# Performance work log

Measured on AMD Instinct MI355X. Metric: run time of the kernel, lower is better.

Reference implementation:

```python
import jax, jax.numpy as jnp
import numpy as np

H = 128
L = 3
N = 100000
E = 1600000
G = 1024
OUT = 10
MAX_LEVEL = 1000
MAX_THOUGHTS = 5000
N_CATE = 5
BN_EPS = 1e-5


def _make_pe(n_pos, h):
    pos = np.arange(n_pos, dtype=np.float32)[:, None]
    div = np.exp(np.arange(0, h, 2, dtype=np.float32) * (-np.log(10000.0) / h))
    pe = np.zeros((n_pos, h), dtype=np.float32)
    pe[:, 0::2] = np.sin(pos * div)
    pe[:, 1::2] = np.cos(pos * div)
    return jnp.asarray(pe)


def setup_inputs() -> dict:
    key = jax.random.key(0)
    ks = jax.random.split(key, 16)
    s = 0.02
    inp = {
        "x": jax.random.randint(ks[0], (N, 3), 0, 5, dtype=jnp.int64 if jax.config.jax_enable_x64 else jnp.int32),
        "edge_index": jax.random.randint(ks[1], (2, E), 0, N),
        "batch": jnp.sort(jax.random.randint(ks[2], (N,), 0, G)),
        "num_graphs": G,
        "pe": _make_pe(MAX_THOUGHTS, H),
        "cate_emb": jax.random.normal(ks[3], (N_CATE, H), jnp.float32) * s,
        "level_emb": jax.random.normal(ks[4], (MAX_LEVEL, H), jnp.float32) * s,
        "conv_W1": jax.random.normal(ks[5], (L, H, H), jnp.float32) * s,
        "conv_b1": jnp.zeros((L, H), jnp.float32),
        "conv_g1": jnp.ones((L, H), jnp.float32),
        "conv_be1": jnp.zeros((L, H), jnp.float32),
        "conv_W2": jax.random.normal(ks[6], (L, H, H), jnp.float32) * s,
        "conv_b2": jnp.zeros((L, H), jnp.float32),
        "norm_g": jnp.ones((L, H), jnp.float32),
        "norm_be": jnp.zeros((L, H), jnp.float32),
        "gate_W1": jax.random.normal(ks[7], (H, H), jnp.float32) * s,
        "gate_b1": jnp.zeros((H,), jnp.float32),
        "gate_W2": jax.random.normal(ks[8], (H, 1), jnp.float32) * s,
        "gate_b2": jnp.zeros((1,), jnp.float32),
        "cls_W1": jax.random.normal(ks[9], (H, H), jnp.float32) * s,
        "cls_b1": jnp.zeros((H,), jnp.float32),
        "cls_g": jnp.ones((H,), jnp.float32),
        "cls_be": jnp.zeros((H,), jnp.float32),
        "cls_W2": jax.random.normal(ks[10], (H, OUT), jnp.float32) * s,
        "cls_b2": jnp.zeros((OUT,), jnp.float32),
    }
    return inp


def _bn(h, g, b):
    # BatchNorm1d, training mode: batch stats over the node/graph dim, biased var
    m = jnp.mean(h, axis=0)
    v = jnp.var(h, axis=0)
    return (h - m) * jax.lax.rsqrt(v + BN_EPS) * g + b


def reference(x, edge_index, batch, num_graphs, pe, cate_emb, level_emb,
              conv_W1, conv_b1, conv_g1, conv_be1, conv_W2, conv_b2,
              norm_g, norm_be, gate_W1, gate_b1, gate_W2, gate_b2,
              cls_W1, cls_b1, cls_g, cls_be, cls_W2, cls_b2):
    # NodeEncoder ('tree'): level + cate + sinusoidal thought PE
    level = jnp.clip(x[:, 0], 0, MAX_LEVEL - 1)
    cate = jnp.clip(x[:, 1], 0, N_CATE - 1)
    thought = jnp.clip(x[:, 2], 0, MAX_THOUGHTS - 1)
    h = cate_emb[cate] + level_emb[level] + pe[thought]  # [N, H]

    src, dst = edge_index[0], edge_index[1]
    n = h.shape[0]
    for i in range(L):
        # GINConv (eps=0): h_i <- MLP(h_i + sum_{j->i} h_j)
        agg = jax.ops.segment_sum(h[src], dst, num_segments=n)
        z = (h + agg) @ conv_W1[i] + conv_b1[i]
        z = jax.nn.relu(_bn(z, conv_g1[i], conv_be1[i]))
        z = z @ conv_W2[i] + conv_b2[i]
        h = jax.nn.relu(_bn(z, norm_g[i], norm_be[i]))

    # GlobalAttention pooling: per-graph softmax over gate scores
    gate = (jax.nn.relu(h @ gate_W1 + gate_b1) @ gate_W2 + gate_b2)[:, 0]  # [N]
    m = jax.ops.segment_max(gate, batch, num_segments=num_graphs)
    e = jnp.exp(gate - m[batch])
    s = jax.ops.segment_sum(e, batch, num_segments=num_graphs)
    alpha = e / s[batch]
    pooled = jax.ops.segment_sum(alpha[:, None] * h, batch, num_segments=num_graphs)  # [G, H]

    # classifier (dropout = 0)
    z = pooled @ cls_W1 + cls_b1
    z = jax.nn.relu(_bn(z, cls_g, cls_be))
    return z @ cls_W2 + cls_b2  # [G, OUT]
```

## Files before the change

### kernel.cpp

```cpp
#include <hip/hip_runtime.h>
#include <math.h>

#define HD 128

typedef __attribute__((ext_vector_type(8))) short bf16x8;
typedef __attribute__((ext_vector_type(4))) unsigned short us4;
typedef __attribute__((ext_vector_type(4))) float f32x4;

__device__ __forceinline__ float bf2f(unsigned short u) {
  union { unsigned int i; float f; } v; v.i = ((unsigned int)u) << 16; return v.f;
}
__device__ __forceinline__ unsigned short f2bf(float f) {
  union { float f; unsigned int i; } v; v.f = f;
  unsigned int u = v.i;
  u += 0x7FFFu + ((u >> 16) & 1u);
  return (unsigned short)(u >> 16);
}

__device__ __forceinline__ void bn_ab(const float* __restrict__ st, const float* __restrict__ g,
                                      const float* __restrict__ be, float inv_n, int c,
                                      float& a, float& b) {
  float s = st[c] + st[256 + c] + st[512 + c] + st[768 + c];
  float sq = st[HD + c] + st[256 + HD + c] + st[512 + HD + c] + st[768 + HD + c];
  float mean = s * inv_n;
  float var = sq * inv_n - mean * mean;
  float inv = rsqrtf(var + 1e-5f);
  a = inv * g[c];
  b = be[c] - mean * a;
}

__global__ void zero_f(float* p, int n) {
  int i = blockIdx.x * blockDim.x + threadIdx.x;
  if (i < n) p[i] = 0.f;
}

__global__ void zero_int(int* p, int n) {
  int stride = gridDim.x * blockDim.x;
  for (int i = blockIdx.x * blockDim.x + threadIdx.x; i < n; i += stride) p[i] = 0;
}

__global__ void encode_kernel(const int* __restrict__ x, const float* __restrict__ pe,
                              const float* __restrict__ ce, const float* __restrict__ le,
                              float* __restrict__ h, unsigned short* __restrict__ hb, int n) {
  int total = n * HD;
  int stride = gridDim.x * blockDim.x;
  for (int idx = blockIdx.x * blockDim.x + threadIdx.x; idx < total; idx += stride) {
    int node = idx >> 7, c = idx & (HD - 1);
    int lv = x[node * 3 + 0]; lv = lv < 0 ? 0 : (lv > 999 ? 999 : lv);
    int ct = x[node * 3 + 1]; ct = ct < 0 ? 0 : (ct > 4 ? 4 : ct);
    int th = x[node * 3 + 2]; th = th < 0 ? 0 : (th > 4999 ? 4999 : th);
    float v = ce[ct * HD + c] + le[lv * HD + c] + pe[th * HD + c];
    h[idx] = v;
    hb[idx] = f2bf(v);
  }
}

__global__ void prep_w(const float* __restrict__ cW1, const float* __restrict__ cW2,
                       const float* __restrict__ gW1,
                       unsigned short* __restrict__ whi, unsigned short* __restrict__ wlo) {
  int m = blockIdx.x;
  const float* W = (m < 3) ? cW1 + (size_t)m * HD * HD
                 : (m < 6) ? cW2 + (size_t)(m - 3) * HD * HD : gW1;
  unsigned short* oh = whi + (size_t)m * HD * HD;
  unsigned short* ol = wlo + (size_t)m * HD * HD;
  for (int i = threadIdx.x; i < HD * HD; i += 256) {
    int j = i & 7;
    int l = (i >> 3) & 63;
    int p = i >> 9;
    int cg = p >> 2, k4 = p & 3;
    int c = cg * 16 + (l & 15);
    int k = (k4 * 4 + (l >> 4)) * 8 + j;
    float f = W[k * HD + c];
    unsigned short hh = f2bf(f);
    oh[i] = hh;
    ol[i] = f2bf(f - bf2f(hh));
  }
}


__global__ void hist_kernel(const int* __restrict__ ei, int* deg, int E, int Wwin) {
  int pass = blockIdx.x & 7;
  int b = blockIdx.x >> 3;
  int tstride = (gridDim.x >> 3) * blockDim.x;
  for (int e = b * blockDim.x + threadIdx.x; e < E; e += tstride) {
    int d = ei[E + e];
    if (d / Wwin == pass) atomicAdd(&deg[d], 1);
  }
}

#define SCAN_BS 1024
__global__ void scan1_kernel(const int* __restrict__ deg, int* __restrict__ off,
                             int* __restrict__ bsum, int n) {
  __shared__ int sh[256];
  int b = blockIdx.x, t = threadIdx.x;
  int base = b * SCAN_BS + t * 4;
  int v[4];
#pragma unroll
  for (int j = 0; j < 4; j++) v[j] = (base + j < n) ? deg[base + j] : 0;
  int s = v[0] + v[1] + v[2] + v[3];
  sh[t] = s;
  __syncthreads();
  for (int o = 1; o < 256; o <<= 1) {
    int x = (t >= o) ? sh[t - o] : 0;
    __syncthreads();
    sh[t] += x;
    __syncthreads();
  }
  int excl = sh[t] - s;
  if (t == 255) bsum[b] = sh[255];
  int run = excl;
#pragma unroll
  for (int j = 0; j < 4; j++) {
    if (base + j < n) off[base + j] = run;
    run += v[j];
  }
}

__global__ void scan2_kernel(int* bsum, int nb) {
  __shared__ int sh[128];
  int t = threadIdx.x;
  int v = (t < nb) ? bsum[t] : 0;
  sh[t] = v;
  __syncthreads();
  for (int o = 1; o < 128; o <<= 1) {
    int x = (t >= o) ? sh[t - o] : 0;
    __syncthreads();
    sh[t] += x;
    __syncthreads();
  }
  if (t < nb) bsum[t] = sh[t] - v;
}

__global__ void scan3_kernel(int* off, int* cursor, const int* __restrict__ bsum,
                             int n, int E) {
  int idx = blockIdx.x * blockDim.x + threadIdx.x;
  int stride = gridDim.x * blockDim.x;
  for (int i = idx; i < n; i += stride) {
    int v = off[i] + bsum[i >> 10];
    off[i] = v;
    cursor[i] = v;
  }
  if (idx == 0) off[n] = E;
}

__global__ void fill_kernel(const int* __restrict__ ei, int* cursor, int* csr_src,
                            int E, int Wwin) {
  int pass = blockIdx.x & 7;
  int b = blockIdx.x >> 3;
  int tstride = (gridDim.x >> 3) * blockDim.x;
  for (int e = b * blockDim.x + threadIdx.x; e < E; e += tstride) {
    int d = ei[E + e];
    if (d / Wwin == pass) {
      int pos = atomicAdd(&cursor[d], 1);
      csr_src[pos] = ei[e];
    }
  }
}

template<bool BN, bool STATS>
__global__ __launch_bounds__(512, 6)
void gemm_gather(const float* __restrict__ h, const unsigned short* __restrict__ hb,
                 const int* __restrict__ off, const int* __restrict__ src,
                 const float* __restrict__ statP, const float* __restrict__ gBN,
                 const float* __restrict__ beBN, float inv_n,
                 const unsigned short* __restrict__ Whi,
                 const unsigned short* __restrict__ Wlo,
                 const float* __restrict__ bias, float* __restrict__ outf,
                 float* __restrict__ statOut, int Nn) {
  __shared__ unsigned short XsH[96 * HD];
  __shared__ unsigned short XsL[96 * HD];
  __shared__ float red[2 * HD];
  __shared__ float abl[2 * HD];
  int t = threadIdx.x;
  long rowbase = (long)blockIdx.x * 96;
  int grp = t >> 5, lane = t & 31;

  if (BN) {
    if (t < HD) {
      float a, b;
      bn_ab(statP, gBN, beBN, inv_n, t, a, b);
      abl[t] = a;
      abl[HD + t] = b;
    }
    __syncthreads();
  }

  float4 a4, b4;
  if (BN) {
    a4 = *(const float4*)(abl + lane * 4);
    b4 = *(const float4*)(abl + HD + lane * 4);
  }
#define APPLY_BN(v) if (BN) { \
    v.x = fmaxf(v.x * a4.x + b4.x, 0.f); \
    v.y = fmaxf(v.y * a4.y + b4.y, 0.f); \
    v.z = fmaxf(v.z * a4.z + b4.z, 0.f); \
    v.w = fmaxf(v.w * a4.w + b4.w, 0.f); }
#define UP4(wv) {bf2f(wv[0]), bf2f(wv[1]), bf2f(wv[2]), bf2f(wv[3])}

  for (int rr = 0; rr < 6; rr++) {
    int r = grp + rr * 16;
    long row = rowbase + r; if (row > Nn - 1) row = Nn - 1;
    int s0 = off[row], s1 = off[row + 1];
    float4 acc0 = *(const float4*)(h + row * HD + lane * 4);
    APPLY_BN(acc0);
    float4 acc1 = {0.f, 0.f, 0.f, 0.f};
    float4 acc2 = {0.f, 0.f, 0.f, 0.f};
    float4 acc3 = {0.f, 0.f, 0.f, 0.f};
    int e = s0;
    for (; e + 8 <= s1; e += 8) {
      int i0 = src[e], i1 = src[e + 1], i2 = src[e + 2], i3 = src[e + 3];
      int i4 = src[e + 4], i5 = src[e + 5], i6 = src[e + 6], i7 = src[e + 7];
      us4 w0 = *(const us4*)(hb + (size_t)i0 * HD + lane * 4);
      us4 w1 = *(const us4*)(hb + (size_t)i1 * HD + lane * 4);
      us4 w2 = *(const us4*)(hb + (size_t)i2 * HD + lane * 4);
      us4 w3 = *(const us4*)(hb + (size_t)i3 * HD + lane * 4);
      us4 w4 = *(const us4*)(hb + (size_t)i4 * HD + lane * 4);
      us4 w5 = *(const us4*)(hb + (size_t)i5 * HD + lane * 4);
      us4 w6 = *(const us4*)(hb + (size_t)i6 * HD + lane * 4);
      us4 w7 = *(const us4*)(hb + (size_t)i7 * HD + lane * 4);
      float4 v0 = UP4(w0), v1 = UP4(w1), v2 = UP4(w2), v3 = UP4(w3);
      float4 v4 = UP4(w4), v5 = UP4(w5), v6 = UP4(w6), v7 = UP4(w7);
      APPLY_BN(v0); APPLY_BN(v1); APPLY_BN(v2); APPLY_BN(v3);
      APPLY_BN(v4); APPLY_BN(v5); APPLY_BN(v6); APPLY_BN(v7);
      acc0.x += v0.x + v4.x; acc0.y += v0.y + v4.y; acc0.z += v0.z + v4.z; acc0.w += v0.w + v4.w;
      acc1.x += v1.x + v5.x; acc1.y += v1.y + v5.y; acc1.z += v1.z + v5.z; acc1.w += v1.w + v5.w;
      acc2.x += v2.x + v6.x; acc2.y += v2.y + v6.y; acc2.z += v2.z + v6.z; acc2.w += v2.w + v6.w;
      acc3.x += v3.x + v7.x; acc3.y += v3.y + v7.y; acc3.z += v3.z + v7.z; acc3.w += v3.w + v7.w;
    }
    for (; e < s1; e++) {
      int s = src[e];
      us4 wv = *(const us4*)(hb + (size_t)s * HD + lane * 4);
      float4 v = UP4(wv);
      APPLY_BN(v);
      acc0.x += v.x; acc0.y += v.y; acc0.z += v.z; acc0.w += v.w;
    }
    acc0.x += acc1.x + acc2.x + acc3.x;
    acc0.y += acc1.y + acc2.y + acc3.y;
    acc0.z += acc1.z + acc2.z + acc3.z;
    acc0.w += acc1.w + acc2.w + acc3.w;
    float f[4] = {acc0.x, acc0.y, acc0.z, acc0.w};
    us4 hi, lo;
#pragma unroll
    for (int j = 0; j < 4; j++) {
      unsigned short hh = f2bf(f[j]);
      hi[j] = hh;
      lo[j] = f2bf(f[j] - bf2f(hh));
    }
    int g8 = lane >> 1;
    int offl = r * HD + (((g8 ^ (r & 7)) << 3)) + (lane & 1) * 4;
    *(us4*)(XsH + offl) = hi;
    *(us4*)(XsL + offl) = lo;
  }
#undef APPLY_BN
#undef UP4
  if (STATS && t < 2 * HD) red[t] = 0.f;
  __syncthreads();

  int w = t >> 6, l = t & 63;
  int lr = l & 15, lg = l >> 4;

  if (w < 6) {
    f32x4 acc[8];
#pragma unroll
    for (int ct = 0; ct < 8; ct++) acc[ct] = (f32x4){0.f, 0.f, 0.f, 0.f};

    bf16x8 aH[4], aL[4];
    int arow = w * 16 + lr;
#pragma unroll
    for (int k4 = 0; k4 < 4; k4++) {
      int kg = k4 * 4 + lg;
      int offa = arow * HD + (((kg ^ (arow & 7)) << 3));
      aH[k4] = *(bf16x8*)(XsH + offa);
      aL[k4] = *(bf16x8*)(XsL + offa);
    }
#pragma unroll
    for (int ct = 0; ct < 8; ct++) {
#pragma unroll
      for (int k4 = 0; k4 < 4; k4++) {
        int bo = (((ct << 2) + k4) * 64 + l) * 8;
        bf16x8 bH = *(const bf16x8*)(Whi + bo);
        bf16x8 bL = *(const bf16x8*)(Wlo + bo);
        acc[ct] = __builtin_amdgcn_mfma_f32_16x16x32_bf16(aH[k4], bH, acc[ct], 0, 0, 0);
        acc[ct] = __builtin_amdgcn_mfma_f32_16x16x32_bf16(aH[k4], bL, acc[ct], 0, 0, 0);
        acc[ct] = __builtin_amdgcn_mfma_f32_16x16x32_bf16(aL[k4], bH, acc[ct], 0, 0, 0);
      }
    }

    float s[8], ss[8];
#pragma unroll
    for (int ct = 0; ct < 8; ct++) { s[ct] = 0.f; ss[ct] = 0.f; }
#pragma unroll
    for (int jj = 0; jj < 4; jj++) {
      long row = rowbase + w * 16 + lg * 4 + jj;
      bool ok = row < Nn;
#pragma unroll
      for (int ct = 0; ct < 8; ct++) {
        float v = acc[ct][jj] + bias[ct * 16 + lr];
        if (ok) {
          outf[row * HD + ct * 16 + lr] = v;
          if (STATS) { s[ct] += v; ss[ct] += v * v; }
        }
      }
    }
    if (STATS) {
#pragma unroll
      for (int ct = 0; ct < 8; ct++) {
        float sv = s[ct], sq = ss[ct];
        sv += __shfl_xor(sv, 16); sq += __shfl_xor(sq, 16);
        sv += __shfl_xor(sv, 32); sq += __shfl_xor(sq, 32);
        if (lg == 0) {
          atomicAdd(&red[ct * 16 + lr], sv);
          atomicAdd(&red[HD + ct * 16 + lr], sq);
        }
      }
    }
  }
  if (STATS) {
    __syncthreads();
    float* st = statOut + (blockIdx.x & 3) * 256;
    if (t < 2 * HD) atomicAdd(&st[t], red[t]);
  }
}

template<bool INBN, bool GATE, bool STATS>
__global__ __launch_bounds__(512, 8)
void gemm_split(const float* __restrict__ X, const unsigned short* __restrict__ Whi,
                const unsigned short* __restrict__ Wlo,
                const float* __restrict__ bias,
                const float* __restrict__ statP, const float* __restrict__ gBN,
                const float* __restrict__ beBN, float inv_n,
                const float* __restrict__ w2, float* __restrict__ outf,
                unsigned short* __restrict__ outb,
                float* __restrict__ gate, float* __restrict__ statOut, int Nn) {
  __shared__ unsigned short XsH[64 * HD];
  __shared__ unsigned short XsL[64 * HD];
  __shared__ float red[2 * HD];
  __shared__ float gred[64];
  __shared__ float abl[2 * HD];
  int t = threadIdx.x;
  long rowbase = (long)blockIdx.x * 64;

  if (INBN) {
    if (t < HD) {
      float a, b;
      bn_ab(statP, gBN, beBN, inv_n, t, a, b);
      abl[t] = a;
      abl[HD + t] = b;
    }
  }
  if (STATS && t < 2 * HD) red[t] = 0.f;
  if (GATE && t < 64) gred[t] = 0.f;
  if (INBN) __syncthreads();

#pragma unroll
  for (int it = 0; it < 4; it++) {
    int i = (t + it * 512) * 4;
    int r = i >> 7, k = i & (HD - 1);
    long row = rowbase + r; if (row > Nn - 1) row = Nn - 1;
    float4 v = *(const float4*)(X + row * HD + k);
    float f[4] = {v.x, v.y, v.z, v.w};
    if (INBN) {
#pragma unroll
      for (int j = 0; j < 4; j++)
        f[j] = fmaxf(f[j] * abl[k + j] + abl[HD + k + j], 0.f);
    }
    us4 hi, lo;
#pragma unroll
    for (int j = 0; j < 4; j++) {
      unsigned short hh = f2bf(f[j]);
      hi[j] = hh;
      lo[j] = f2bf(f[j] - bf2f(hh));
    }
    int g = k >> 3;
    int off = r * HD + ((((g ^ (r & 7)) << 3)) | (k & 7));
    *(us4*)(XsH + off) = hi;
    *(us4*)(XsL + off) = lo;
  }
  __syncthreads();

  int w = t >> 6, l = t & 63;
  int lr = l & 15, lg = l >> 4;
  int wr = w & 3, wc = w >> 2;

  f32x4 acc[4];
#pragma unroll
  for (int ct = 0; ct < 4; ct++) acc[ct] = (f32x4){0.f, 0.f, 0.f, 0.f};

  bf16x8 aH[4], aL[4];
  int arow = wr * 16 + lr;
#pragma unroll
  for (int k4 = 0; k4 < 4; k4++) {
    int kg = k4 * 4 + lg;
    int off = arow * HD + (((kg ^ (arow & 7)) << 3));
    aH[k4] = *(bf16x8*)(XsH + off);
    aL[k4] = *(bf16x8*)(XsL + off);
  }
#pragma unroll
  for (int ct = 0; ct < 4; ct++) {
    int cg = wc * 4 + ct;
#pragma unroll
    for (int k4 = 0; k4 < 4; k4++) {
      int bo = (((cg << 2) + k4) * 64 + l) * 8;
      bf16x8 bH = *(const bf16x8*)(Whi + bo);
      bf16x8 bL = *(const bf16x8*)(Wlo + bo);
      acc[ct] = __builtin_amdgcn_mfma_f32_16x16x32_bf16(aH[k4], bH, acc[ct], 0, 0, 0);
      acc[ct] = __builtin_amdgcn_mfma_f32_16x16x32_bf16(aH[k4], bL, acc[ct], 0, 0, 0);
      acc[ct] = __builtin_amdgcn_mfma_f32_16x16x32_bf16(aL[k4], bH, acc[ct], 0, 0, 0);
    }
  }

  if (GATE) {
#pragma unroll
    for (int jj = 0; jj < 4; jj++) {
      float p = 0.f;
#pragma unroll
      for (int ct = 0; ct < 4; ct++) {
        int col = (wc * 4 + ct) * 16 + lr;
        float v = fmaxf(acc[ct][jj] + bias[col], 0.f);
        p += v * w2[col];
      }
      p += __shfl_xor(p, 1);
      p += __shfl_xor(p, 2);
      p += __shfl_xor(p, 4);
      p += __shfl_xor(p, 8);
      if (lr == 0) atomicAdd(&gred[wr * 16 + lg * 4 + jj], p);
    }
    __syncthreads();
    if (t < 64 && rowbase + t < Nn) gate[rowbase + t] = gred[t];
  } else {
    float s[4], ss[4];
#pragma unroll
    for (int ct = 0; ct < 4; ct++) { s[ct] = 0.f; ss[ct] = 0.f; }
#pragma unroll
    for (int jj = 0; jj < 4; jj++) {
      long row = rowbase + wr * 16 + lg * 4 + jj;
      bool ok = row < Nn;
#pragma unroll
      for (int ct = 0; ct < 4; ct++) {
        int col = (wc * 4 + ct) * 16 + lr;
        float v = acc[ct][jj] + bias[col];
        if (ok) {
          outf[row * HD + col] = v;
          if (outb) outb[row * HD + col] = f2bf(v);
          if (STATS) { s[ct] += v; ss[ct] += v * v; }
        }
      }
    }
    if (STATS) {
#pragma unroll
      for (int ct = 0; ct < 4; ct++) {
        int col = (wc * 4 + ct) * 16 + lr;
        float sv = s[ct], sq = ss[ct];
        sv += __shfl_xor(sv, 16); sq += __shfl_xor(sq, 16);
        sv += __shfl_xor(sv, 32); sq += __shfl_xor(sq, 32);
        if (lg == 0) {
          atomicAdd(&red[col], sv);
          atomicAdd(&red[HD + col], sq);
        }
      }
      __syncthreads();
      float* st = statOut + (blockIdx.x & 3) * 256;
      if (t < 2 * HD) atomicAdd(&st[t], red[t]);
    }
  }
}

__global__ void bound_kernel(const int* __restrict__ batch, int* gs, int N, int G) {
  int i = blockIdx.x * blockDim.x + threadIdx.x;
  if (i >= N) return;
  int b = batch[i];
  int prev = (i == 0) ? -1 : batch[i - 1];
  for (int g = prev + 1; g <= b; g++) gs[g] = i;
  if (i == N - 1)
    for (int g = b + 1; g <= G; g++) gs[g] = N;
}

__global__ void fused_pool(const float* __restrict__ h, const float* __restrict__ gate,
                           const int* __restrict__ gs,
                           const float* __restrict__ statP, const float* __restrict__ gBN,
                           const float* __restrict__ beBN, float inv_n,
                           float* __restrict__ pooled) {
  int g = blockIdx.x;
  int t = threadIdx.x;
  int s0 = gs[g], s1 = gs[g + 1];
  if (s0 >= s1) { pooled[(size_t)g * HD + t] = 0.f; return; }
  __shared__ float red[HD];
  float a, b;
  bn_ab(statP, gBN, beBN, inv_n, t, a, b);
  float m = -INFINITY;
  for (int i = s0 + t; i < s1; i += HD) m = fmaxf(m, gate[i]);
  red[t] = m;
  __syncthreads();
  for (int o = 64; o > 0; o >>= 1) {
    if (t < o) red[t] = fmaxf(red[t], red[t + o]);
    __syncthreads();
  }
  m = red[0];
  __syncthreads();
  float s = 0.f;
  for (int i = s0 + t; i < s1; i += HD) s += expf(gate[i] - m);
  red[t] = s;
  __syncthreads();
  for (int o = 64; o > 0; o >>= 1) {
    if (t < o) red[t] += red[t + o];
    __syncthreads();
  }
  float inv = 1.f / red[0];
  float acc = 0.f;
  int i = s0;
  for (; i + 4 <= s1; i += 4) {
    float al0 = expf(gate[i] - m);
    float al1 = expf(gate[i + 1] - m);
    float al2 = expf(gate[i + 2] - m);
    float al3 = expf(gate[i + 3] - m);
    float v0 = fmaxf(h[(size_t)(i + 0) * HD + t] * a + b, 0.f);
    float v1 = fmaxf(h[(size_t)(i + 1) * HD + t] * a + b, 0.f);
    float v2 = fmaxf(h[(size_t)(i + 2) * HD + t] * a + b, 0.f);
    float v3 = fmaxf(h[(size_t)(i + 3) * HD + t] * a + b, 0.f);
    acc += al0 * v0 + al1 * v1 + al2 * v2 + al3 * v3;
  }
  for (; i < s1; i++) {
    float al = expf(gate[i] - m);
    float v = fmaxf(h[(size_t)i * HD + t] * a + b, 0.f);
    acc += al * v;
  }
  pooled[(size_t)g * HD + t] = acc * inv;
}

__global__ __launch_bounds__(256, 4)
void gemm_f32(const float* __restrict__ X, const float* __restrict__ W,
              const float* __restrict__ bias, float* __restrict__ out, int Nn) {
  __shared__ float XsT[32][132];
  __shared__ float Ws[32][HD];
  int t = threadIdx.x;
  int r0 = (t >> 4) * 8;
  int c0 = (t & 15) * 8;
  long rowbase = (long)blockIdx.x * 128;

  float acc[8][8];
#pragma unroll
  for (int ci = 0; ci < 8; ci++) {
    float bv = bias[c0 + ci];
#pragma unroll
    for (int ri = 0; ri < 8; ri++) acc[ri][ci] = bv;
  }

  int sr = t >> 1;
  int hf = t & 1;
  long srow = rowbase + sr; if (srow > Nn - 1) srow = Nn - 1;
  const float* xrow = X + srow * HD;

  for (int k0 = 0; k0 < HD; k0 += 32) {
    __syncthreads();
#pragma unroll
    for (int j = 0; j < 4; j++) {
      int i = j * 1024 + t * 4;
      int kk = i >> 7, c = i & (HD - 1);
      *(float4*)&Ws[kk][c] = *(const float4*)&W[(size_t)(k0 + kk) * HD + c];
    }
#pragma unroll
    for (int j = 0; j < 4; j++) {
      int kc = k0 + hf * 16 + j * 4;
      float4 v = *(const float4*)&xrow[kc];
      int kl = hf * 16 + j * 4;
      XsT[kl + 0][sr] = v.x;
      XsT[kl + 1][sr] = v.y;
      XsT[kl + 2][sr] = v.z;
      XsT[kl + 3][sr] = v.w;
    }
    __syncthreads();
#pragma unroll 8
    for (int kk = 0; kk < 32; kk++) {
      float4 a0 = *(float4*)&XsT[kk][r0];
      float4 a1 = *(float4*)&XsT[kk][r0 + 4];
      float4 b0 = *(float4*)&Ws[kk][c0];
      float4 b1 = *(float4*)&Ws[kk][c0 + 4];
      float ar[8] = {a0.x, a0.y, a0.z, a0.w, a1.x, a1.y, a1.z, a1.w};
      float bc[8] = {b0.x, b0.y, b0.z, b0.w, b1.x, b1.y, b1.z, b1.w};
#pragma unroll
      for (int ri = 0; ri < 8; ri++)
#pragma unroll
        for (int ci = 0; ci < 8; ci++) acc[ri][ci] += ar[ri] * bc[ci];
    }
  }

#pragma unroll
  for (int ri = 0; ri < 8; ri++) {
    long row = rowbase + r0 + ri;
    if (row < Nn) {
      float4 o0 = {acc[ri][0], acc[ri][1], acc[ri][2], acc[ri][3]};
      float4 o1 = {acc[ri][4], acc[ri][5], acc[ri][6], acc[ri][7]};
      *(float4*)&out[row * HD + c0] = o0;
      *(float4*)&out[row * HD + c0 + 4] = o1;
    }
  }
}

__global__ void stats_f32(const float* __restrict__ z, float* stat, int n) {
  int c = threadIdx.x & (HD - 1);
  int rg = threadIdx.x >> 7;
  float s = 0.f, ss = 0.f;
  for (int r = blockIdx.x * 2 + rg; r < n; r += gridDim.x * 2) {
    float v = z[(size_t)r * HD + c];
    s += v; ss += v * v;
  }
  __shared__ float S[2][HD], SS[2][HD];
  S[rg][c] = s; SS[rg][c] = ss;
  __syncthreads();
  if (threadIdx.x < HD) {
    atomicAdd(&stat[c], S[0][c] + S[1][c]);
    atomicAdd(&stat[HD + c], SS[0][c] + SS[1][c]);
  }
}

__global__ void cls_out_kernel(const float* __restrict__ zc, const float* __restrict__ stat,
                               const float* __restrict__ g, const float* __restrict__ be,
                               float inv_n, const float* __restrict__ W2,
                               const float* __restrict__ b2, float* out, int G) {
  int row = blockIdx.x;
  int t = threadIdx.x;
  float mean0 = stat[t] * inv_n;
  float var0 = stat[HD + t] * inv_n - mean0 * mean0;
  float a0 = rsqrtf(var0 + 1e-5f) * g[t];
  float b0 = be[t] - mean0 * a0;
  float mean1 = stat[64 + t] * inv_n;
  float var1 = stat[HD + 64 + t] * inv_n - mean1 * mean1;
  float a1 = rsqrtf(var1 + 1e-5f) * g[64 + t];
  float b1 = be[64 + t] - mean1 * a1;
  float v0 = fmaxf(zc[(size_t)row * HD + t] * a0 + b0, 0.f);
  float v1 = fmaxf(zc[(size_t)row * HD + 64 + t] * a1 + b1, 0.f);
  for (int o = 0; o < 10; o++) {
    float p = v0 * W2[t * 10 + o] + v1 * W2[(64 + t) * 10 + o];
#pragma unroll
    for (int s = 32; s > 0; s >>= 1) p += __shfl_down(p, s);
    if (t == 0) out[row * 10 + o] = p + b2[o];
  }
}

extern "C" void kernel_launch(void* const* d_in, const int* in_sizes, int n_in,
                              void* d_out, int out_size, void* d_ws, size_t ws_size,
                              hipStream_t stream) {
  const int* x     = (const int*)d_in[0];
  const int* ei    = (const int*)d_in[1];
  const int* batch = (const int*)d_in[2];
  const float* pe  = (const float*)d_in[4];
  const float* ce  = (const float*)d_in[5];
  const float* le  = (const float*)d_in[6];
  const float* cW1 = (const float*)d_in[7];
  const float* cb1 = (const float*)d_in[8];
  const float* cg1 = (const float*)d_in[9];
  const float* cbe1= (const float*)d_in[10];
  const float* cW2 = (const float*)d_in[11];
  const float* cb2 = (const float*)d_in[12];
  const float* ngm = (const float*)d_in[13];
  const float* nbe = (const float*)d_in[14];
  const float* gW1 = (const float*)d_in[15];
  const float* gb1 = (const float*)d_in[16];
  const float* gW2 = (const float*)d_in[17];
  const float* clW1= (const float*)d_in[19];
  const float* clb1= (const float*)d_in[20];
  const float* clg = (const float*)d_in[21];
  const float* clbe= (const float*)d_in[22];
  const float* clW2= (const float*)d_in[23];
  const float* clb2= (const float*)d_in[24];

  int N = in_sizes[2];
  int E = in_sizes[1] / 2;
  int G = out_size / 10;

  float* buf0   = (float*)d_ws;
  float* buf1   = buf0 + (size_t)N * HD;
  float* pooled = buf1 + (size_t)N * HD;
  float* gate   = pooled + (size_t)G * HD;
  float* zc     = gate + N;
  float* stats  = zc + (size_t)G * HD;
  unsigned short* whi = (unsigned short*)(stats + 7 * 1024);
  unsigned short* wlo = whi + 7 * HD * HD;
  unsigned short* hbb = wlo + 7 * HD * HD;
  int* csr_off  = (int*)(hbb + (size_t)N * HD);
  int* cursor   = csr_off + (N + 1);
  int* bsum     = cursor + N;
  int* gs       = bsum + 128;
  int* csr_src  = gs + (G + 1);

  float* out = (float*)d_out;
  int gatherBlocks = (N + 95) / 96;
  int splitBlocks  = (N + 63) / 64;
  int Wwin = (N + 7) / 8;
  float invN = 1.f / N;

  zero_f<<<28, 256, 0, stream>>>(stats, 7 * 1024);
  encode_kernel<<<2048, 256, 0, stream>>>(x, pe, ce, le, buf0, hbb, N);
  prep_w<<<7, 256, 0, stream>>>(cW1, cW2, gW1, whi, wlo);

  int nb = (N + SCAN_BS - 1) / SCAN_BS;
  zero_int<<<256, 256, 0, stream>>>(cursor, N);
  hist_kernel<<<2048, 256, 0, stream>>>(ei, cursor, E, Wwin);
  scan1_kernel<<<nb, 256, 0, stream>>>(cursor, csr_off, bsum, N);
  scan2_kernel<<<1, 128, 0, stream>>>(bsum, nb);
  scan3_kernel<<<256, 256, 0, stream>>>(csr_off, cursor, bsum, N, E);
  fill_kernel<<<2048, 256, 0, stream>>>(ei, cursor, csr_src, E, Wwin);
  bound_kernel<<<(N + 255) / 256, 256, 0, stream>>>(batch, gs, N, G);

  for (int l = 0; l < 3; l++) {
    const float* statPrev = stats + (l - 1) * 2048 + 1024;
    if (l == 0)
      gemm_gather<false, true><<<gatherBlocks, 512, 0, stream>>>(
          buf0, hbb, csr_off, csr_src, nullptr, nullptr, nullptr, invN,
          whi + (size_t)l * HD * HD, wlo + (size_t)l * HD * HD,
          cb1 + l * HD, buf1, stats + l * 2048, N);
    else
      gemm_gather<true, true><<<gatherBlocks, 512, 0, stream>>>(
          buf0, hbb, csr_off, csr_src, statPrev, ngm + (l - 1) * HD, nbe + (l - 1) * HD, invN,
          whi + (size_t)l * HD * HD, wlo + (size_t)l * HD * HD,
          cb1 + l * HD, buf1, stats + l * 2048, N);
    gemm_split<true, false, true><<<splitBlocks, 512, 0, stream>>>(
        buf1, whi + (size_t)(3 + l) * HD * HD, wlo + (size_t)(3 + l) * HD * HD,
        cb2 + l * HD, stats + l * 2048, cg1 + l * HD, cbe1 + l * HD, invN,
        nullptr, buf0, (l < 2) ? hbb : nullptr, nullptr, stats + l * 2048 + 1024, N);
  }

  const float* statFin = stats + 2 * 2048 + 1024;
  gemm_split<true, true, false><<<splitBlocks, 512, 0, stream>>>(
      buf0, whi + (size_t)6 * HD * HD, wlo + (size_t)6 * HD * HD,
      gb1, statFin, ngm + 2 * HD, nbe + 2 * HD, invN,
      gW2, nullptr, nullptr, gate, nullptr, N);
  fused_pool<<<G, HD, 0, stream>>>(buf0, gate, gs, statFin, ngm + 2 * HD, nbe + 2 * HD,
                                   invN, pooled);

  gemm_f32<<<(G + 127) / 128, 256, 0, stream>>>(pooled, clW1, clb1, zc, G);
  stats_f32<<<64, 256, 0, stream>>>(zc, stats + 6 * 1024, G);
  cls_out_kernel<<<G, 64, 0, stream>>>(zc, stats + 6 * 1024, clg, clbe, 1.f / G,
                                       clW2, clb2, out, G);
}
```

Before: 756.5 us.

## Split fused gather+GEMM into standalone gather kernel followed by gemm_split

The fused kernel that gathered neighbour sums into LDS and then ran the first MLP GEMM is replaced by two kernels. A grid-stride gather kernel writes the fp32 aggregate to a global buffer, and the existing gemm_split kernel then runs the GEMM in place on that buffer and collects the BN statistics. The aim is to let the latency-bound gather run without the LDS and launch-bounds limits of the GEMM, so more gathers can be in flight. The cost is an extra fp32 write and read of an N×128 buffer per layer, plus one more launch per layer. The in-place GEMM output also relies on each block reading its rows before it writes them.

New measurement: 769.1 us. Within noise of the previous version (+1.7%).

```diff
diff --git a/kernel.cpp b/kernel.cpp
--- a/kernel.cpp
+++ b/kernel.cpp
@@ -157,38 +157,21 @@
   }
 }
 
-template<bool BN, bool STATS>
-__global__ __launch_bounds__(512, 6)
-void gemm_gather(const float* __restrict__ h, const unsigned short* __restrict__ hb,
-                 const int* __restrict__ off, const int* __restrict__ src,
-                 const float* __restrict__ statP, const float* __restrict__ gBN,
-                 const float* __restrict__ beBN, float inv_n,
-                 const unsigned short* __restrict__ Whi,
-                 const unsigned short* __restrict__ Wlo,
-                 const float* __restrict__ bias, float* __restrict__ outf,
-                 float* __restrict__ statOut, int Nn) {
-  __shared__ unsigned short XsH[96 * HD];
-  __shared__ unsigned short XsL[96 * HD];
-  __shared__ float red[2 * HD];
-  __shared__ float abl[2 * HD];
-  int t = threadIdx.x;
-  long rowbase = (long)blockIdx.x * 96;
-  int grp = t >> 5, lane = t & 31;
-
-  if (BN) {
-    if (t < HD) {
-      float a, b;
-      bn_ab(statP, gBN, beBN, inv_n, t, a, b);
-      abl[t] = a;
-      abl[HD + t] = b;
-    }
-    __syncthreads();
-  }
-
+template<bool BN>
+__global__ void gather_kernel(const float* __restrict__ h, const unsigned short* __restrict__ hb,
+                              const int* __restrict__ off, const int* __restrict__ src,
+                              const float* __restrict__ statP, const float* __restrict__ gBN,
+                              const float* __restrict__ beBN, float inv_n,
+                              float* __restrict__ out, int N) {
+  int gid = (blockIdx.x * blockDim.x + threadIdx.x) >> 5;
+  int lane = threadIdx.x & 31;
+  int ng = (gridDim.x * blockDim.x) >> 5;
   float4 a4, b4;
   if (BN) {
-    a4 = *(const float4*)(abl + lane * 4);
-    b4 = *(const float4*)(abl + HD + lane * 4);
+    bn_ab(statP, gBN, beBN, inv_n, lane * 4 + 0, a4.x, b4.x);
+    bn_ab(statP, gBN, beBN, inv_n, lane * 4 + 1, a4.y, b4.y);
+    bn_ab(statP, gBN, beBN, inv_n, lane * 4 + 2, a4.z, b4.z);
+    bn_ab(statP, gBN, beBN, inv_n, lane * 4 + 3, a4.w, b4.w);
   }
 #define APPLY_BN(v) if (BN) { \
     v.x = fmaxf(v.x * a4.x + b4.x, 0.f); \
@@ -196,12 +179,9 @@
     v.z = fmaxf(v.z * a4.z + b4.z, 0.f); \
     v.w = fmaxf(v.w * a4.w + b4.w, 0.f); }
 #define UP4(wv) {bf2f(wv[0]), bf2f(wv[1]), bf2f(wv[2]), bf2f(wv[3])}
-
-  for (int rr = 0; rr < 6; rr++) {
-    int r = grp + rr * 16;
-    long row = rowbase + r; if (row > Nn - 1) row = Nn - 1;
-    int s0 = off[row], s1 = off[row + 1];
-    float4 acc0 = *(const float4*)(h + row * HD + lane * 4);
+  for (int i = gid; i < N; i += ng) {
+    int s0 = off[i], s1 = off[i + 1];
+    float4 acc0 = *(const float4*)(h + (size_t)i * HD + lane * 4);
     APPLY_BN(acc0);
     float4 acc1 = {0.f, 0.f, 0.f, 0.f};
     float4 acc2 = {0.f, 0.f, 0.f, 0.f};
@@ -238,88 +218,10 @@
     acc0.y += acc1.y + acc2.y + acc3.y;
     acc0.z += acc1.z + acc2.z + acc3.z;
     acc0.w += acc1.w + acc2.w + acc3.w;
-    float f[4] = {acc0.x, acc0.y, acc0.z, acc0.w};
-    us4 hi, lo;
-#pragma unroll
-    for (int j = 0; j < 4; j++) {
-      unsigned short hh = f2bf(f[j]);
-      hi[j] = hh;
-      lo[j] = f2bf(f[j] - bf2f(hh));
-    }
-    int g8 = lane >> 1;
-    int offl = r * HD + (((g8 ^ (r & 7)) << 3)) + (lane & 1) * 4;
-    *(us4*)(XsH + offl) = hi;
-    *(us4*)(XsL + offl) = lo;
+    *(float4*)(out + (size_t)i * HD + lane * 4) = acc0;
   }
 #undef APPLY_BN
 #undef UP4
-  if (STATS && t < 2 * HD) red[t] = 0.f;
-  __syncthreads();
-
-  int w = t >> 6, l = t & 63;
-  int lr = l & 15, lg = l >> 4;
-
-  if (w < 6) {
-    f32x4 acc[8];
-#pragma unroll
-    for (int ct = 0; ct < 8; ct++) acc[ct] = (f32x4){0.f, 0.f, 0.f, 0.f};
-
-    bf16x8 aH[4], aL[4];
-    int arow = w * 16 + lr;
-#pragma unroll
-    for (int k4 = 0; k4 < 4; k4++) {
-      int kg = k4 * 4 + lg;
-      int offa = arow * HD + (((kg ^ (arow & 7)) << 3));
-      aH[k4] = *(bf16x8*)(XsH + offa);
-      aL[k4] = *(bf16x8*)(XsL + offa);
-    }
-#pragma unroll
-    for (int ct = 0; ct < 8; ct++) {
-#pragma unroll
-      for (int k4 = 0; k4 < 4; k4++) {
-        int bo = (((ct << 2) + k4) * 64 + l) * 8;
-        bf16x8 bH = *(const bf16x8*)(Whi + bo);
-        bf16x8 bL = *(const bf16x8*)(Wlo + bo);
-        acc[ct] = __builtin_amdgcn_mfma_f32_16x16x32_bf16(aH[k4], bH, acc[ct], 0, 0, 0);
-        acc[ct] = __builtin_amdgcn_mfma_f32_16x16x32_bf16(aH[k4], bL, acc[ct], 0, 0, 0);
-        acc[ct] = __builtin_amdgcn_mfma_f32_16x16x32_bf16(aL[k4], bH, acc[ct], 0, 0, 0);
-      }
-    }
-
-    float s[8], ss[8];
-#pragma unroll
-    for (int ct = 0; ct < 8; ct++) { s[ct] = 0.f; ss[ct] = 0.f; }
-#pragma unroll
-    for (int jj = 0; jj < 4; jj++) {
-      long row = rowbase + w * 16 + lg * 4 + jj;
-      bool ok = row < Nn;
-#pragma unroll
-      for (int ct = 0; ct < 8; ct++) {
-        float v = acc[ct][jj] + bias[ct * 16 + lr];
-        if (ok) {
-          outf[row * HD + ct * 16 + lr] = v;
-          if (STATS) { s[ct] += v; ss[ct] += v * v; }
-        }
-      }
-    }
-    if (STATS) {
-#pragma unroll
-      for (int ct = 0; ct < 8; ct++) {
-        float sv = s[ct], sq = ss[ct];
-        sv += __shfl_xor(sv, 16); sq += __shfl_xor(sq, 16);
-        sv += __shfl_xor(sv, 32); sq += __shfl_xor(sq, 32);
-        if (lg == 0) {
-          atomicAdd(&red[ct * 16 + lr], sv);
-          atomicAdd(&red[HD + ct * 16 + lr], sq);
-        }
-      }
-    }
-  }
-  if (STATS) {
-    __syncthreads();
-    float* st = statOut + (blockIdx.x & 3) * 256;
-    if (t < 2 * HD) atomicAdd(&st[t], red[t]);
-  }
 }
 
 template<bool INBN, bool GATE, bool STATS>
@@ -684,7 +586,6 @@
   int* csr_src  = gs + (G + 1);
 
   float* out = (float*)d_out;
-  int gatherBlocks = (N + 95) / 96;
   int splitBlocks  = (N + 63) / 64;
   int Wwin = (N + 7) / 8;
   float invN = 1.f / N;
@@ -705,15 +606,16 @@
   for (int l = 0; l < 3; l++) {
     const float* statPrev = stats + (l - 1) * 2048 + 1024;
     if (l == 0)
-      gemm_gather<false, true><<<gatherBlocks, 512, 0, stream>>>(
-          buf0, hbb, csr_off, csr_src, nullptr, nullptr, nullptr, invN,
-          whi + (size_t)l * HD * HD, wlo + (size_t)l * HD * HD,
-          cb1 + l * HD, buf1, stats + l * 2048, N);
+      gather_kernel<false><<<2048, 256, 0, stream>>>(
+          buf0, hbb, csr_off, csr_src, nullptr, nullptr, nullptr, invN, buf1, N);
     else
-      gemm_gather<true, true><<<gatherBlocks, 512, 0, stream>>>(
-          buf0, hbb, csr_off, csr_src, statPrev, ngm + (l - 1) * HD, nbe + (l - 1) * HD, invN,
-          whi + (size_t)l * HD * HD, wlo + (size_t)l * HD * HD,
-          cb1 + l * HD, buf1, stats + l * 2048, N);
+      gather_kernel<true><<<2048, 256, 0, stream>>>(
+          buf0, hbb, csr_off, csr_src, statPrev, ngm + (l - 1) * HD, nbe + (l - 1) * HD,
+          invN, buf1, N);
+    gemm_split<false, false, true><<<splitBlocks, 512, 0, stream>>>(
+        buf1, whi + (size_t)l * HD * HD, wlo + (size_t)l * HD * HD,
+        cb1 + l * HD, nullptr, nullptr, nullptr, invN,
+        nullptr, buf1, nullptr, nullptr, stats + l * 2048, N);
     gemm_split<true, false, true><<<splitBlocks, 512, 0, stream>>>(
         buf1, whi + (size_t)(3 + l) * HD * HD, wlo + (size_t)(3 + l) * HD * HD,
         cb2 + l * HD, stats + l * 2048, cg1 + l * HD, cbe1 + l * HD, invN,
```
